# Performance work log

Measured on AMD Instinct MI355X. Metric: run time of the kernel, lower is better.

The kernel has to match this reference:

```python
import jax, jax.numpy as jnp
import numpy as np

NUM_HEADS = 12
SIZE_PER_HEAD = 64
NEG_INF = -10000.0


def setup_inputs() -> dict:
    key = jax.random.key(0)
    k1, k2, k3, k4 = jax.random.split(key, 4)
    B, S, D = 2, 2048, 768
    x = jax.random.normal(k1, (B, S, D), dtype=jnp.float32)
    mask = jax.random.randint(k2, (B, S, S), 0, 2, dtype=jnp.int32)
    std = 0.02
    Wq = jax.random.normal(k3, (D, NUM_HEADS * SIZE_PER_HEAD), dtype=jnp.float32) * std
    Wk = jax.random.normal(k4, (D, NUM_HEADS * SIZE_PER_HEAD), dtype=jnp.float32) * std
    bq = jnp.zeros((NUM_HEADS * SIZE_PER_HEAD,), dtype=jnp.float32)
    bk = jnp.zeros((NUM_HEADS * SIZE_PER_HEAD,), dtype=jnp.float32)
    return {"x": x, "mask": mask, "Wq": Wq, "bq": bq, "Wk": Wk, "bk": bk}


def reference(x, mask, Wq, bq, Wk, bk):
    B, S, D = x.shape
    H, dh = NUM_HEADS, SIZE_PER_HEAD
    # Dense query/key projections (no activation), then split heads: [B,H,S,dh]
    q = (x @ Wq + bq).reshape(B, S, H, dh).transpose(0, 2, 1, 3)
    k = (x @ Wk + bk).reshape(B, S, H, dh).transpose(0, 2, 1, 3)
    # Scaled dot-product scores: [B,H,S,S]
    scores = jnp.einsum("bhqd,bhkd->bhqk", q, k) / jnp.sqrt(jnp.float32(dh))
    # Mask: [B,S,S] -> [B,1,S,S]; zeros get large negative additive bias
    adder = (1.0 - mask.astype(jnp.float32))[:, None, :, :] * NEG_INF
    probs = jax.nn.softmax(scores + adder, axis=-1)
    # dropout is identity at inference (training=None)
    return probs
```

## Files before the change

### kernel.cpp

```cpp
#include <hip/hip_runtime.h>
#include <stdint.h>

#define NUM_HEADS 12
#define DH 64
#define SEQ 2048
#define BATCH 2
#define DM 768
#define NQK 1536
#define LOG2E 1.44269504088896340736f

typedef short short8 __attribute__((ext_vector_type(8)));
typedef short short4_t __attribute__((ext_vector_type(4)));
typedef float f32x4 __attribute__((ext_vector_type(4)));

__device__ __forceinline__ short bf16_rne(float f) {
    union { float f; uint32_t u; } v; v.f = f;
    return (short)((v.u + 0x7FFFu + ((v.u >> 16) & 1u)) >> 16);
}

__global__ __launch_bounds__(256) void wt_kernel(const float* __restrict__ Wq,
                                                 const float* __restrict__ Wk,
                                                 short* __restrict__ Wt) {
    __shared__ float tile[32][33];
    int n0 = blockIdx.x * 32;
    int k0 = blockIdx.y * 32;
    int tx = threadIdx.x & 31;
    int ty = threadIdx.x >> 5;
    const float* src = (n0 < DM) ? Wq : Wk;
    int nn0 = (n0 < DM) ? n0 : n0 - DM;
#pragma unroll
    for (int j = 0; j < 4; ++j) {
        int k = ty + 8 * j;
        tile[k][tx] = src[(size_t)(k0 + k) * DM + nn0 + tx];
    }
    __syncthreads();
#pragma unroll
    for (int j = 0; j < 4; ++j) {
        int n = ty + 8 * j;
        Wt[(size_t)(n0 + n) * DM + k0 + tx] = bf16_rne(tile[tx][n]);
    }
}

__global__ __launch_bounds__(256) void xb_kernel(const float* __restrict__ x,
                                                 short* __restrict__ Xb) {
    int i = (blockIdx.x * 256 + threadIdx.x) * 4;
    f32x4 v = *(const f32x4*)(x + i);
    short4_t s;
#pragma unroll
    for (int j = 0; j < 4; ++j) s[j] = bf16_rne(v[j]);
    *(short4_t*)(Xb + i) = s;
}

__global__ __launch_bounds__(256) void mpack_kernel(const int* __restrict__ mask,
                                                    unsigned long long* __restrict__ Mb) {
    int wid = (blockIdx.x * 256 + threadIdx.x) >> 6;
    int lane = threadIdx.x & 63;
    size_t base = (size_t)wid * 8;
#pragma unroll
    for (int i = 0; i < 8; ++i) {
        size_t w = base + i;
        int v = mask[w * 64 + lane];
        unsigned long long bal = __ballot(v != 0);
        if (lane == 0) Mb[w] = bal;
    }
}

__global__ __launch_bounds__(256) void proj_kernel(const short* __restrict__ Xb,
                                                   const short* __restrict__ Wt,
                                                   const float* __restrict__ bq,
                                                   const float* __restrict__ bk,
                                                   short* __restrict__ QK) {
    __shared__ short As[2][128 * 40];
    __shared__ short Bs[2][64 * 40];
    const int m0 = blockIdx.x * 128;
    const int n0 = blockIdx.y * 64;
    const int t = threadIdx.x;
    const int lane = t & 63;
    const int w = t >> 6;
    const int wr = w >> 1, wc = w & 1;
    const int lr = lane & 15;
    const int lk = lane >> 4;

    const int ar0 = t >> 2, ach = t & 3;
    const int br0 = t >> 2, bch = t & 3;

    f32x4 acc[4][2] = {};
    short8 ra0, ra1, rb;

#define PROJ_LOAD(K0)                                                              \
    ra0 = *(const short8*)&Xb[(size_t)(m0 + ar0) * DM + (K0) + ach * 8];           \
    ra1 = *(const short8*)&Xb[(size_t)(m0 + ar0 + 64) * DM + (K0) + ach * 8];      \
    rb  = *(const short8*)&Wt[(size_t)(n0 + br0) * DM + (K0) + bch * 8];

#define PROJ_WRITE(BUF)                                                            \
    *(short8*)&As[BUF][ar0 * 40 + ach * 8] = ra0;                                  \
    *(short8*)&As[BUF][(ar0 + 64) * 40 + ach * 8] = ra1;                           \
    *(short8*)&Bs[BUF][br0 * 40 + bch * 8] = rb;

    PROJ_LOAD(0)
    PROJ_WRITE(0)
    __syncthreads();

    int cur = 0;
    for (int s = 0; s < DM / 32; ++s) {
        if (s < DM / 32 - 1) { PROJ_LOAD((s + 1) * 32) }
        short8 a[4], bb[2];
#pragma unroll
        for (int m = 0; m < 4; ++m)
            a[m] = *(short8*)&As[cur][(wr * 64 + m * 16 + lr) * 40 + lk * 8];
#pragma unroll
        for (int n = 0; n < 2; ++n)
            bb[n] = *(short8*)&Bs[cur][(wc * 32 + n * 16 + lr) * 40 + lk * 8];
#pragma unroll
        for (int m = 0; m < 4; ++m)
#pragma unroll
            for (int n = 0; n < 2; ++n)
                acc[m][n] = __builtin_amdgcn_mfma_f32_16x16x32_bf16(a[m], bb[n], acc[m][n], 0, 0, 0);
        if (s < DM / 32 - 1) { PROJ_WRITE(cur ^ 1) }
        __syncthreads();
        cur ^= 1;
    }

    const int orow = m0 + wr * 64;
    const int ocol = n0 + wc * 32;
#pragma unroll
    for (int m = 0; m < 4; ++m) {
#pragma unroll
        for (int n = 0; n < 2; ++n) {
            int col = ocol + n * 16 + lr;
            float bias = (col < DM) ? bq[col] : bk[col - DM];
            float scale = (col < DM) ? 0.125f * LOG2E : 1.0f;
#pragma unroll
            for (int r = 0; r < 4; ++r) {
                int row = orow + m * 16 + lk * 4 + r;
                QK[(size_t)row * NQK + col] = bf16_rne((acc[m][n][r] + bias) * scale);
            }
        }
    }
#undef PROJ_LOAD
#undef PROJ_WRITE
}

__global__ __launch_bounds__(256) void attn_kernel(const short* __restrict__ QK,
                                                   const unsigned long long* __restrict__ Mb,
                                                   float* __restrict__ out) {
    __shared__ short Ks[2][64 * 72];
    const int qblk = blockIdx.x;
    const int h = blockIdx.y;
    const int b = blockIdx.z;
    const int t = threadIdx.x;
    const int lane = t & 63;
    const int w = t >> 6;
    const int lr = lane & 15;
    const int lk = lane >> 4;
    const int wq = qblk * 64 + w * 16;
    const int q = wq + lr;

    short8 aq0 = *(const short8*)&QK[(size_t)(b * SEQ + q) * NQK + h * DH + lk * 8];
    short8 aq1 = *(const short8*)&QK[(size_t)(b * SEQ + q) * NQK + h * DH + 32 + lk * 8];

    const size_t mrow = (size_t)b * SEQ * (SEQ / 64) + (size_t)q * 32;
    const int srow = t >> 3, sch = t & 7;
    short8 rs0, rs1;

#define ATT_LOAD(KT)                                                                          \
    rs0 = *(const short8*)&QK[(size_t)(b * SEQ + (KT) + srow) * NQK + DM + h * DH + sch * 8]; \
    rs1 = *(const short8*)&QK[(size_t)(b * SEQ + (KT) + srow + 32) * NQK + DM + h * DH + sch * 8];

#define ATT_WRITE(BUF)                                                                        \
    *(short8*)&Ks[BUF][srow * 72 + sch * 8] = rs0;                                            \
    *(short8*)&Ks[BUF][(srow + 32) * 72 + sch * 8] = rs1;

    float lsum = 0.0f;
    ATT_LOAD(0)
    ATT_WRITE(0)
    __syncthreads();
    int cur = 0;
    for (int kt = 0; kt < SEQ; kt += 64) {
        if (kt + 64 < SEQ) { ATT_LOAD(kt + 64) }
        unsigned long long mbs = Mb[mrow + (kt >> 6)] >> (lk * 4);
#pragma unroll
        for (int nf = 0; nf < 4; ++nf) {
            short8 k0 = *(short8*)&Ks[cur][(nf * 16 + lr) * 72 + lk * 8];
            short8 k1 = *(short8*)&Ks[cur][(nf * 16 + lr) * 72 + 32 + lk * 8];
            f32x4 a = {0.f, 0.f, 0.f, 0.f};
            a = __builtin_amdgcn_mfma_f32_16x16x32_bf16(k0, aq0, a, 0, 0, 0);
            a = __builtin_amdgcn_mfma_f32_16x16x32_bf16(k1, aq1, a, 0, 0, 0);
#pragma unroll
            for (int r = 0; r < 4; ++r) {
                float e = __builtin_amdgcn_exp2f(a[r]);
                lsum += ((mbs >> (nf * 16 + r)) & 1ull) ? e : 0.f;
            }
        }
        if (kt + 64 < SEQ) { ATT_WRITE(cur ^ 1) }
        __syncthreads();
        cur ^= 1;
    }

    lsum += __shfl_xor(lsum, 16, 64);
    lsum += __shfl_xor(lsum, 32, 64);
    float li = -__log2f(lsum);
    f32x4 li4 = {li, li, li, li};

    const size_t orow = ((size_t)((b * NUM_HEADS + h) * SEQ) + q) * SEQ;
    ATT_LOAD(0)
    ATT_WRITE(0)
    __syncthreads();
    cur = 0;
    for (int kt = 0; kt < SEQ; kt += 64) {
        if (kt + 64 < SEQ) { ATT_LOAD(kt + 64) }
        unsigned long long mbs = Mb[mrow + (kt >> 6)] >> (lk * 4);
#pragma unroll
        for (int nf = 0; nf < 4; ++nf) {
            short8 k0 = *(short8*)&Ks[cur][(nf * 16 + lr) * 72 + lk * 8];
            short8 k1 = *(short8*)&Ks[cur][(nf * 16 + lr) * 72 + 32 + lk * 8];
            f32x4 a = __builtin_amdgcn_mfma_f32_16x16x32_bf16(k0, aq0, li4, 0, 0, 0);
            a = __builtin_amdgcn_mfma_f32_16x16x32_bf16(k1, aq1, a, 0, 0, 0);
            f32x4 p;
#pragma unroll
            for (int r = 0; r < 4; ++r) {
                float e = __builtin_amdgcn_exp2f(a[r]);
                p[r] = ((mbs >> (nf * 16 + r)) & 1ull) ? e : 0.f;
            }
            *(f32x4*)&out[orow + kt + nf * 16 + lk * 4] = p;
        }
        if (kt + 64 < SEQ) { ATT_WRITE(cur ^ 1) }
        __syncthreads();
        cur ^= 1;
    }
#undef ATT_LOAD
#undef ATT_WRITE
}

extern "C" void kernel_launch(void* const* d_in, const int* in_sizes, int n_in,
                              void* d_out, int out_size, void* d_ws, size_t ws_size,
                              hipStream_t stream) {
    (void)in_sizes; (void)n_in; (void)out_size; (void)ws_size;
    const float* x = (const float*)d_in[0];
    const int* mask = (const int*)d_in[1];
    const float* Wq = (const float*)d_in[2];
    const float* bq = (const float*)d_in[3];
    const float* Wk = (const float*)d_in[4];
    const float* bk = (const float*)d_in[5];
    float* out = (float*)d_out;

    short* Wt = (short*)d_ws;
    short* Xb = Wt + (size_t)NQK * DM;
    short* QK = Xb + (size_t)BATCH * SEQ * DM;
    unsigned long long* Mb =
        (unsigned long long*)(QK + (size_t)BATCH * SEQ * NQK);

    wt_kernel<<<dim3(NQK / 32, DM / 32), 256, 0, stream>>>(Wq, Wk, Wt);
    xb_kernel<<<dim3((BATCH * SEQ * DM) / (256 * 4)), 256, 0, stream>>>(x, Xb);
    mpack_kernel<<<dim3((BATCH * SEQ * SEQ / 64) / 32), 256, 0, stream>>>(mask, Mb);
    proj_kernel<<<dim3(BATCH * SEQ / 128, NQK / 64), 256, 0, stream>>>(Xb, Wt, bq, bk, QK);
    attn_kernel<<<dim3(SEQ / 64, NUM_HEADS, BATCH), 256, 0, stream>>>(QK, Mb, out);
}
```

Baseline: 186.7 us.

## Enlarge projection and attention tiles to reuse K and weight loads across more rows

The projection GEMM tile grows from 128x64 to 128x128, and its double-buffered prefetch is replaced by a simpler single-buffer load/sync loop. The attention kernel now has each wave handle 32 queries (two 16-row fragments) instead of 16, so every K tile staged in shared memory feeds twice as many MFMAs and the number of blocks is halved. This is meant to cut redundant K/weight traffic and barrier overhead. In exchange, register pressure and occupancy suffer, the grid becomes smaller, and the projection loses its load/compute overlap.

```diff
diff --git a/kernel.cpp b/kernel.cpp
--- a/kernel.cpp
+++ b/kernel.cpp
@@ -70,10 +70,10 @@
                                                    const float* __restrict__ bq,
                                                    const float* __restrict__ bk,
                                                    short* __restrict__ QK) {
-    __shared__ short As[2][128 * 40];
-    __shared__ short Bs[2][64 * 40];
+    __shared__ short As[128 * 40];
+    __shared__ short Bs[128 * 40];
     const int m0 = blockIdx.x * 128;
-    const int n0 = blockIdx.y * 64;
+    const int n0 = blockIdx.y * 128;
     const int t = threadIdx.x;
     const int lane = t & 63;
     const int w = t >> 6;
@@ -81,52 +81,41 @@
     const int lr = lane & 15;
     const int lk = lane >> 4;
 
-    const int ar0 = t >> 2, ach = t & 3;
-    const int br0 = t >> 2, bch = t & 3;
-
-    f32x4 acc[4][2] = {};
-    short8 ra0, ra1, rb;
-
-#define PROJ_LOAD(K0)                                                              \
-    ra0 = *(const short8*)&Xb[(size_t)(m0 + ar0) * DM + (K0) + ach * 8];           \
-    ra1 = *(const short8*)&Xb[(size_t)(m0 + ar0 + 64) * DM + (K0) + ach * 8];      \
-    rb  = *(const short8*)&Wt[(size_t)(n0 + br0) * DM + (K0) + bch * 8];
-
-#define PROJ_WRITE(BUF)                                                            \
-    *(short8*)&As[BUF][ar0 * 40 + ach * 8] = ra0;                                  \
-    *(short8*)&As[BUF][(ar0 + 64) * 40 + ach * 8] = ra1;                           \
-    *(short8*)&Bs[BUF][br0 * 40 + bch * 8] = rb;
-
-    PROJ_LOAD(0)
-    PROJ_WRITE(0)
-    __syncthreads();
-
-    int cur = 0;
-    for (int s = 0; s < DM / 32; ++s) {
-        if (s < DM / 32 - 1) { PROJ_LOAD((s + 1) * 32) }
-        short8 a[4], bb[2];
+    f32x4 acc[4][4] = {};
+
+    for (int k0 = 0; k0 < DM; k0 += 32) {
+#pragma unroll
+        for (int j = 0; j < 2; ++j) {
+            int idx = t + 256 * j;
+            int row = idx >> 2;
+            int ch = idx & 3;
+            *(short8*)&As[row * 40 + ch * 8] =
+                *(const short8*)&Xb[(size_t)(m0 + row) * DM + k0 + ch * 8];
+            *(short8*)&Bs[row * 40 + ch * 8] =
+                *(const short8*)&Wt[(size_t)(n0 + row) * DM + k0 + ch * 8];
+        }
+        __syncthreads();
+        short8 a[4], bfr[4];
 #pragma unroll
         for (int m = 0; m < 4; ++m)
-            a[m] = *(short8*)&As[cur][(wr * 64 + m * 16 + lr) * 40 + lk * 8];
-#pragma unroll
-        for (int n = 0; n < 2; ++n)
-            bb[n] = *(short8*)&Bs[cur][(wc * 32 + n * 16 + lr) * 40 + lk * 8];
+            a[m] = *(short8*)&As[(wr * 64 + m * 16 + lr) * 40 + lk * 8];
+#pragma unroll
+        for (int n = 0; n < 4; ++n)
+            bfr[n] = *(short8*)&Bs[(wc * 64 + n * 16 + lr) * 40 + lk * 8];
 #pragma unroll
         for (int m = 0; m < 4; ++m)
 #pragma unroll
-            for (int n = 0; n < 2; ++n)
-                acc[m][n] = __builtin_amdgcn_mfma_f32_16x16x32_bf16(a[m], bb[n], acc[m][n], 0, 0, 0);
-        if (s < DM / 32 - 1) { PROJ_WRITE(cur ^ 1) }
-        __syncthreads();
-        cur ^= 1;
+            for (int n = 0; n < 4; ++n)
+                acc[m][n] = __builtin_amdgcn_mfma_f32_16x16x32_bf16(a[m], bfr[n], acc[m][n], 0, 0, 0);
+        __syncthreads();
     }
 
     const int orow = m0 + wr * 64;
-    const int ocol = n0 + wc * 32;
+    const int ocol = n0 + wc * 64;
 #pragma unroll
     for (int m = 0; m < 4; ++m) {
 #pragma unroll
-        for (int n = 0; n < 2; ++n) {
+        for (int n = 0; n < 4; ++n) {
             int col = ocol + n * 16 + lr;
             float bias = (col < DM) ? bq[col] : bk[col - DM];
             float scale = (col < DM) ? 0.125f * LOG2E : 1.0f;
@@ -137,8 +126,6 @@
             }
         }
     }
-#undef PROJ_LOAD
-#undef PROJ_WRITE
 }
 
 __global__ __launch_bounds__(256) void attn_kernel(const short* __restrict__ QK,
@@ -153,13 +140,20 @@
     const int w = t >> 6;
     const int lr = lane & 15;
     const int lk = lane >> 4;
-    const int wq = qblk * 64 + w * 16;
-    const int q = wq + lr;
-
-    short8 aq0 = *(const short8*)&QK[(size_t)(b * SEQ + q) * NQK + h * DH + lk * 8];
-    short8 aq1 = *(const short8*)&QK[(size_t)(b * SEQ + q) * NQK + h * DH + 32 + lk * 8];
-
-    const size_t mrow = (size_t)b * SEQ * (SEQ / 64) + (size_t)q * 32;
+    const int wq = qblk * 128 + w * 32;
+
+    short8 aq[2][2];
+#pragma unroll
+    for (int qf = 0; qf < 2; ++qf)
+#pragma unroll
+        for (int ks = 0; ks < 2; ++ks)
+            aq[qf][ks] = *(const short8*)&QK[(size_t)(b * SEQ + wq + qf * 16 + lr) * NQK +
+                                             h * DH + ks * 32 + lk * 8];
+
+    const size_t mrow[2] = {
+        (size_t)b * SEQ * (SEQ / 64) + (size_t)(wq + lr) * 32,
+        (size_t)b * SEQ * (SEQ / 64) + (size_t)(wq + 16 + lr) * 32};
+
     const int srow = t >> 3, sch = t & 7;
     short8 rs0, rs1;
 
@@ -171,25 +165,31 @@
     *(short8*)&Ks[BUF][srow * 72 + sch * 8] = rs0;                                            \
     *(short8*)&Ks[BUF][(srow + 32) * 72 + sch * 8] = rs1;
 
-    float lsum = 0.0f;
+    float lsum[2] = {0.f, 0.f};
     ATT_LOAD(0)
     ATT_WRITE(0)
     __syncthreads();
     int cur = 0;
     for (int kt = 0; kt < SEQ; kt += 64) {
         if (kt + 64 < SEQ) { ATT_LOAD(kt + 64) }
-        unsigned long long mbs = Mb[mrow + (kt >> 6)] >> (lk * 4);
+        unsigned long long mb0 = Mb[mrow[0] + (kt >> 6)] >> (lk * 4);
+        unsigned long long mb1 = Mb[mrow[1] + (kt >> 6)] >> (lk * 4);
 #pragma unroll
         for (int nf = 0; nf < 4; ++nf) {
             short8 k0 = *(short8*)&Ks[cur][(nf * 16 + lr) * 72 + lk * 8];
             short8 k1 = *(short8*)&Ks[cur][(nf * 16 + lr) * 72 + 32 + lk * 8];
-            f32x4 a = {0.f, 0.f, 0.f, 0.f};
-            a = __builtin_amdgcn_mfma_f32_16x16x32_bf16(k0, aq0, a, 0, 0, 0);
-            a = __builtin_amdgcn_mfma_f32_16x16x32_bf16(k1, aq1, a, 0, 0, 0);
+            f32x4 a0 = {0.f, 0.f, 0.f, 0.f};
+            a0 = __builtin_amdgcn_mfma_f32_16x16x32_bf16(k0, aq[0][0], a0, 0, 0, 0);
+            a0 = __builtin_amdgcn_mfma_f32_16x16x32_bf16(k1, aq[0][1], a0, 0, 0, 0);
+            f32x4 a1 = {0.f, 0.f, 0.f, 0.f};
+            a1 = __builtin_amdgcn_mfma_f32_16x16x32_bf16(k0, aq[1][0], a1, 0, 0, 0);
+            a1 = __builtin_amdgcn_mfma_f32_16x16x32_bf16(k1, aq[1][1], a1, 0, 0, 0);
 #pragma unroll
             for (int r = 0; r < 4; ++r) {
-                float e = __builtin_amdgcn_exp2f(a[r]);
-                lsum += ((mbs >> (nf * 16 + r)) & 1ull) ? e : 0.f;
+                float e0 = __builtin_amdgcn_exp2f(a0[r]);
+                float e1 = __builtin_amdgcn_exp2f(a1[r]);
+                lsum[0] += ((mb0 >> (nf * 16 + r)) & 1ull) ? e0 : 0.f;
+                lsum[1] += ((mb1 >> (nf * 16 + r)) & 1ull) ? e1 : 0.f;
             }
         }
         if (kt + 64 < SEQ) { ATT_WRITE(cur ^ 1) }
@@ -197,32 +197,45 @@
         cur ^= 1;
     }
 
-    lsum += __shfl_xor(lsum, 16, 64);
-    lsum += __shfl_xor(lsum, 32, 64);
-    float li = -__log2f(lsum);
-    f32x4 li4 = {li, li, li, li};
-
-    const size_t orow = ((size_t)((b * NUM_HEADS + h) * SEQ) + q) * SEQ;
+    f32x4 li4[2];
+#pragma unroll
+    for (int qf = 0; qf < 2; ++qf) {
+        float l = lsum[qf];
+        l += __shfl_xor(l, 16, 64);
+        l += __shfl_xor(l, 32, 64);
+        float li = -__log2f(l);
+        li4[qf] = (f32x4){li, li, li, li};
+    }
+
+    const size_t orow[2] = {
+        ((size_t)((b * NUM_HEADS + h) * SEQ) + wq + lr) * SEQ,
+        ((size_t)((b * NUM_HEADS + h) * SEQ) + wq + 16 + lr) * SEQ};
     ATT_LOAD(0)
     ATT_WRITE(0)
     __syncthreads();
     cur = 0;
     for (int kt = 0; kt < SEQ; kt += 64) {
         if (kt + 64 < SEQ) { ATT_LOAD(kt + 64) }
-        unsigned long long mbs = Mb[mrow + (kt >> 6)] >> (lk * 4);
+        unsigned long long mb0 = Mb[mrow[0] + (kt >> 6)] >> (lk * 4);
+        unsigned long long mb1 = Mb[mrow[1] + (kt >> 6)] >> (lk * 4);
 #pragma unroll
         for (int nf = 0; nf < 4; ++nf) {
             short8 k0 = *(short8*)&Ks[cur][(nf * 16 + lr) * 72 + lk * 8];
             short8 k1 = *(short8*)&Ks[cur][(nf * 16 + lr) * 72 + 32 + lk * 8];
-            f32x4 a = __builtin_amdgcn_mfma_f32_16x16x32_bf16(k0, aq0, li4, 0, 0, 0);
-            a = __builtin_amdgcn_mfma_f32_16x16x32_bf16(k1, aq1, a, 0, 0, 0);
-            f32x4 p;
+            f32x4 a0 = __builtin_amdgcn_mfma_f32_16x16x32_bf16(k0, aq[0][0], li4[0], 0, 0, 0);
+            a0 = __builtin_amdgcn_mfma_f32_16x16x32_bf16(k1, aq[0][1], a0, 0, 0, 0);
+            f32x4 a1 = __builtin_amdgcn_mfma_f32_16x16x32_bf16(k0, aq[1][0], li4[1], 0, 0, 0);
+            a1 = __builtin_amdgcn_mfma_f32_16x16x32_bf16(k1, aq[1][1], a1, 0, 0, 0);
+            f32x4 p0, p1;
 #pragma unroll
             for (int r = 0; r < 4; ++r) {
-                float e = __builtin_amdgcn_exp2f(a[r]);
-                p[r] = ((mbs >> (nf * 16 + r)) & 1ull) ? e : 0.f;
+                float e0 = __builtin_amdgcn_exp2f(a0[r]);
+                float e1 = __builtin_amdgcn_exp2f(a1[r]);
+                p0[r] = ((mb0 >> (nf * 16 + r)) & 1ull) ? e0 : 0.f;
+                p1[r] = ((mb1 >> (nf * 16 + r)) & 1ull) ? e1 : 0.f;
             }
-            *(f32x4*)&out[orow + kt + nf * 16 + lk * 4] = p;
+            *(f32x4*)&out[orow[0] + kt + nf * 16 + lk * 4] = p0;
+            *(f32x4*)&out[orow[1] + kt + nf * 16 + lk * 4] = p1;
         }
         if (kt + 64 < SEQ) { ATT_WRITE(cur ^ 1) }
         __syncthreads();
@@ -253,6 +266,6 @@
     wt_kernel<<<dim3(NQK / 32, DM / 32), 256, 0, stream>>>(Wq, Wk, Wt);
     xb_kernel<<<dim3((BATCH * SEQ * DM) / (256 * 4)), 256, 0, stream>>>(x, Xb);
     mpack_kernel<<<dim3((BATCH * SEQ * SEQ / 64) / 32), 256, 0, stream>>>(mask, Mb);
-    proj_kernel<<<dim3(BATCH * SEQ / 128, NQK / 64), 256, 0, stream>>>(Xb, Wt, bq, bk, QK);
-    attn_kernel<<<dim3(SEQ / 64, NUM_HEADS, BATCH), 256, 0, stream>>>(QK, Mb, out);
-}
+    proj_kernel<<<dim3(BATCH * SEQ / 128, NQK / 128), 256, 0, stream>>>(Xb, Wt, bq, bk, QK);
+    attn_kernel<<<dim3(SEQ / 128, NUM_HEADS, BATCH), 256, 0, stream>>>(QK, Mb, out);
+}
```

Result: slower. 220.7 us (+18.2%).
